# Kernel tuning notes

Measured on AMD Instinct MI355X. Metric: run time of the kernel, lower is better.

Reference implementation:

```python
import jax, jax.numpy as jnp
import numpy as np

N_NODES = 100000
E2 = 1600000
E3 = 1600000
ES = 100000
HID = 64


def _mlp_3x3(x_in, W1, b1, W2, b2):
    # x_in: [E, d_in] -> mobility [E, 3, 3]
    h = jax.nn.relu(x_in @ W1 + b1)
    out = h @ W2 + b2  # [E, 9]
    return out.reshape(-1, 3, 3)


def setup_inputs() -> dict:
    key = jax.random.key(0)
    ks = jax.random.split(key, 20)
    inp = {}
    inp["x"] = jax.random.normal(ks[0], (N_NODES, 3), dtype=jnp.float32)
    inp["edge_2body"] = jax.random.randint(ks[1], (2, E2), 0, N_NODES)
    inp["edge_3body"] = jax.random.randint(ks[2], (3, E3), 0, N_NODES)
    inp["edge_2bodySelf"] = jax.random.randint(ks[3], (2, ES), 0, N_NODES)
    inp["edge_1body"] = jax.random.randint(ks[4], (2, ES), 0, N_NODES)
    inp["edge_attr_2body"] = jax.random.normal(ks[5], (E2, 3), dtype=jnp.float32)
    inp["edge_attr_3body"] = jax.random.normal(ks[6], (E3, 3), dtype=jnp.float32)
    inp["edge_attr_2bodySelf"] = jax.random.normal(ks[7], (ES, 3), dtype=jnp.float32)
    inp["edge_attr_1body"] = jax.random.normal(ks[8], (ES, 3), dtype=jnp.float32)
    s = 0.1
    # nn_2body: 3 -> HID -> 9
    inp["W1_2b"] = jax.random.normal(ks[9], (3, HID), dtype=jnp.float32) * s
    inp["b1_2b"] = jnp.zeros((HID,), jnp.float32)
    inp["W2_2b"] = jax.random.normal(ks[10], (HID, 9), dtype=jnp.float32) * s
    inp["b2_2b"] = jnp.zeros((9,), jnp.float32)
    # nn_3body: 6 -> HID -> 9
    inp["W1_3b"] = jax.random.normal(ks[11], (6, HID), dtype=jnp.float32) * s
    inp["b1_3b"] = jnp.zeros((HID,), jnp.float32)
    inp["W2_3b"] = jax.random.normal(ks[12], (HID, 9), dtype=jnp.float32) * s
    inp["b2_3b"] = jnp.zeros((9,), jnp.float32)
    # nn_self: 3 -> HID -> 9
    inp["W1_s"] = jax.random.normal(ks[13], (3, HID), dtype=jnp.float32) * s
    inp["b1_s"] = jnp.zeros((HID,), jnp.float32)
    inp["W2_s"] = jax.random.normal(ks[14], (HID, 9), dtype=jnp.float32) * s
    inp["b2_s"] = jnp.zeros((9,), jnp.float32)
    return inp


def reference(x, edge_2body, edge_3body, edge_2bodySelf, edge_1body,
              edge_attr_2body, edge_attr_3body, edge_attr_2bodySelf, edge_attr_1body,
              W1_2b, b1_2b, W2_2b, b2_2b,
              W1_3b, b1_3b, W2_3b, b2_3b,
              W1_s, b1_s, W2_s, b2_s):
    n = x.shape[0]
    # ---- 2-body: gather -> MLP -> per-edge 3x3 matvec -> scatter-add ----
    d2 = x[edge_2body[0]] - x[edge_2body[1]]  # xj - xi, [E2,3]
    mob2 = _mlp_3x3(d2, W1_2b, b1_2b, W2_2b, b2_2b)
    y2 = jnp.einsum('eij,ej->ei', mob2, edge_attr_2body)
    v2 = jax.ops.segment_sum(y2, edge_2body[1], num_segments=n)
    # ---- 3-body ----
    xj = x[edge_3body[0]]
    xk = x[edge_3body[1]]
    xi = x[edge_3body[2]]
    d3 = jnp.concatenate((xk - xj, xi - xk), axis=1)  # [E3,6]
    mob3 = _mlp_3x3(d3, W1_3b, b1_3b, W2_3b, b2_3b)
    y3 = jnp.einsum('eij,ej->ei', mob3, edge_attr_3body)
    v3 = jax.ops.segment_sum(y3, edge_3body[2], num_segments=n)
    # ---- 2-body self ----
    ds = x[edge_2bodySelf[0]] - x[edge_2bodySelf[1]]
    mobs = _mlp_3x3(ds, W1_s, b1_s, W2_s, b2_s)
    ys = jnp.einsum('eij,ej->ei', mobs, edge_attr_2bodySelf)
    vs = jax.ops.segment_sum(ys, edge_2bodySelf[1], num_segments=n)
    # edge_1body / edge_attr_1body unused in original forward
    return v2 + v3 + vs
```

## Files before the change

kernel.cpp:

```cpp
#include <hip/hip_runtime.h>


constexpr int HIDDEN = 64;
constexpr int NB_MAX = 256;
constexpr int NPB_SHIFT = 9;
constexpr int NPB = 1 << NPB_SHIFT;
constexpr int TILE_F = NPB * 3;
constexpr int NET_SLOT = 1040;

typedef _Float16 h2_t __attribute__((ext_vector_type(2)));

__device__ __forceinline__ unsigned packh2(float a, float b) {
    auto h = __builtin_amdgcn_cvt_pkrtz(a, b);
    return __builtin_bit_cast(unsigned, h);
}
__device__ __forceinline__ float fdot2u(unsigned a, unsigned b, float c) {
    h2_t ha = __builtin_bit_cast(h2_t, a);
    h2_t hb = __builtin_bit_cast(h2_t, b);
#if __has_builtin(__builtin_amdgcn_fdot2)
    return __builtin_amdgcn_fdot2(ha, hb, c, false);
#else
    return fmaf((float)ha.x, (float)hb.x, fmaf((float)ha.y, (float)hb.y, c));
#endif
}


__global__ __launch_bounds__(256) void setup_kernel(
    const float* __restrict__ x, int n_nodes, float4* __restrict__ x4,
    int* __restrict__ gcount,
    const float* __restrict__ W1_2b, const float* __restrict__ b1_2b,
    const float* __restrict__ W2_2b, const float* __restrict__ b2_2b,
    const float* __restrict__ W1_s,  const float* __restrict__ b1_s,
    const float* __restrict__ W2_s,  const float* __restrict__ b2_s,
    const float* __restrict__ W1_3b, const float* __restrict__ b1_3b,
    const float* __restrict__ W2_3b, const float* __restrict__ b2_3b,
    unsigned* __restrict__ nets)
{
    const int blk = blockIdx.x;
    const int tid = threadIdx.x;
    if (blk < 3) {
        const float *W1, *b1, *W2, *b2; int din;
        if (blk == 0) { W1 = W1_2b; b1 = b1_2b; W2 = W2_2b; b2 = b2_2b; din = 3; }
        else if (blk == 1) { W1 = W1_s; b1 = b1_s; W2 = W2_s; b2 = b2_s; din = 3; }
        else { W1 = W1_3b; b1 = b1_3b; W2 = W2_3b; b2 = b2_3b; din = 6; }
        unsigned* slot = nets + blk * NET_SLOT;
        float* slotf = (float*)slot;
        if (tid < 32) {
            const int h2 = tid, hA = 2 * h2, hB = 2 * h2 + 1;
            if (din == 3) {
                unsigned* row = slot + h2 * 16;
                float* rowf = (float*)row;
                row[0] = packh2(W1[0 * HIDDEN + hA], W1[1 * HIDDEN + hA]);
                row[1] = packh2(W1[0 * HIDDEN + hB], W1[1 * HIDDEN + hB]);
                rowf[2] = b1[hA]; rowf[3] = b1[hB];
                rowf[4] = W1[2 * HIDDEN + hA]; rowf[5] = W1[2 * HIDDEN + hB];
                #pragma unroll
                for (int i = 0; i < 9; ++i)
                    row[6 + i] = packh2(W2[hA * 9 + i], W2[hB * 9 + i]);
                row[15] = 0;
            } else {
                unsigned* row = slot + h2 * 32;
                float* rowf = (float*)row;
                #pragma unroll
                for (int r = 0; r < 3; ++r) {
                    row[r]     = packh2(W1[(2 * r) * HIDDEN + hA], W1[(2 * r + 1) * HIDDEN + hA]);
                    row[3 + r] = packh2(W1[(2 * r) * HIDDEN + hB], W1[(2 * r + 1) * HIDDEN + hB]);
                }
                rowf[6] = b1[hA]; rowf[7] = b1[hB];
                #pragma unroll
                for (int i = 0; i < 9; ++i)
                    row[8 + i] = packh2(W2[hA * 9 + i], W2[hB * 9 + i]);
                #pragma unroll
                for (int i = 17; i < 20; ++i) row[i] = 0;
            }
        }
        if (tid >= 32 && tid < 41) slotf[1024 + (tid - 32)] = b2[tid - 32];
        if (blk == 0) gcount[tid] = 0;
    } else {
        int i = (blk - 3) * 256 + tid;
        if (i < n_nodes)
            x4[i] = make_float4(x[3 * i], x[3 * i + 1], x[3 * i + 2], 0.0f);
    }
}

__global__ __launch_bounds__(256) void p1_edge_kernel(
    const float4* __restrict__ x4,
    const int* __restrict__ e0, long long E0, const float* __restrict__ at0,
    const int* __restrict__ e1, long long E1, const float* __restrict__ at1,
    const int* __restrict__ e2, long long E2, const float* __restrict__ at2,
    int g0, int g1,
    const unsigned* __restrict__ nets,
    float4* __restrict__ records, int* __restrict__ gcount, int cap)
{
    constexpr int BLK = 256;
    constexpr int KPT = 4;
    static_assert(NB_MAX == BLK, "one reserve bin per thread");

    __shared__ int s_hist[NB_MAX];
    __shared__ int s_base[NB_MAX];
    __shared__ int s_rank[NB_MAX];

    const int gA = g0 + g1;
    const int gB = (int)gridDim.x - gA;
    const int mn = (gA < gB) ? gA : gB;
    int aidx = -1, b6 = -1;
    {
        const int idx = blockIdx.x;
        if (idx < 2 * mn) { if (idx & 1) b6 = idx >> 1; else aidx = idx >> 1; }
        else {
            const int r = idx - 2 * mn;
            if (gA > gB) aidx = mn + r; else b6 = mn + r;
        }
    }

    const int* edges; long long E; const float* attr;
    int bidx, nblk, din3;
    const unsigned* wp;
    if (aidx >= 0) {
        if (aidx < g0) { edges = e0; E = E0; attr = at0; bidx = aidx;      nblk = g0; din3 = 1; wp = nets; }
        else           { edges = e1; E = E1; attr = at1; bidx = aidx - g0; nblk = g1; din3 = 1; wp = nets + NET_SLOT; }
    } else             { edges = e2; E = E2; attr = at2; bidx = b6;        nblk = gB; din3 = 0; wp = nets + 2 * NET_SLOT; }

    const int tid = threadIdx.x;
    long long span = (E + nblk - 1) / nblk;
    span = (span + 1023) & ~1023LL;
    const long long lo = (long long)bidx * span;
    const long long hi = (lo + span < E) ? (lo + span) : E;
    if (lo >= E) return;

    const bool e_aligned = ((E & 3) == 0);

    const float* b2f = (const float*)(wp + 1024);
    float b2r[9];
    #pragma unroll
    for (int i = 0; i < 9; ++i) b2r[i] = b2f[i];

    for (int i = tid; i < NB_MAX; i += BLK) { s_hist[i] = 0; s_rank[i] = 0; }
    __syncthreads();

    const long long dstrow = din3 ? E : 2 * E;
    for (long long t0 = lo; t0 < hi; t0 += BLK * KPT) {
        const long long be = t0 + (long long)tid * KPT;
        if (be >= hi) continue;
        if (e_aligned && be + KPT <= hi) {
            int4 r = *(const int4*)(edges + dstrow + be);
            atomicAdd(&s_hist[r.x >> NPB_SHIFT], 1);
            atomicAdd(&s_hist[r.y >> NPB_SHIFT], 1);
            atomicAdd(&s_hist[r.z >> NPB_SHIFT], 1);
            atomicAdd(&s_hist[r.w >> NPB_SHIFT], 1);
        } else {
            #pragma unroll
            for (int u = 0; u < KPT; ++u) {
                long long e = be + u;
                if (e < hi)
                    atomicAdd(&s_hist[edges[dstrow + e] >> NPB_SHIFT], 1);
            }
        }
    }
    __syncthreads();

    int my_base = 0;
    {
        const int h = s_hist[tid];
        if (h > 0) my_base = atomicAdd(&gcount[tid], h);
    }

    bool first = true;
    for (long long t0 = lo; t0 < hi; t0 += BLK * KPT) {
        const long long be = t0 + (long long)tid * KPT;

        unsigned dp[KPT][3];
        float    d2s[KPT];
        float    a[KPT][3];
        int      dst[KPT];
        bool     valid[KPT];
        int      i0[KPT], i1[KPT], i2[KPT];

        const bool full = e_aligned && (be + KPT <= hi);
        if (full) {
            int4 r0 = *(const int4*)(edges + be);
            int4 r1 = *(const int4*)(edges + E + be);
            i0[0] = r0.x; i0[1] = r0.y; i0[2] = r0.z; i0[3] = r0.w;
            i1[0] = r1.x; i1[1] = r1.y; i1[2] = r1.z; i1[3] = r1.w;
            if (!din3) {
                int4 r2 = *(const int4*)(edges + 2 * E + be);
                i2[0] = r2.x; i2[1] = r2.y; i2[2] = r2.z; i2[3] = r2.w;
            }
            float4 a0 = *(const float4*)(attr + 3 * be);
            float4 a1 = *(const float4*)(attr + 3 * be + 4);
            float4 a2 = *(const float4*)(attr + 3 * be + 8);
            a[0][0] = a0.x; a[0][1] = a0.y; a[0][2] = a0.z;
            a[1][0] = a0.w; a[1][1] = a1.x; a[1][2] = a1.y;
            a[2][0] = a1.z; a[2][1] = a1.w; a[2][2] = a2.x;
            a[3][0] = a2.y; a[3][1] = a2.z; a[3][2] = a2.w;
            #pragma unroll
            for (int u = 0; u < KPT; ++u) valid[u] = true;
        } else {
            #pragma unroll
            for (int u = 0; u < KPT; ++u) {
                long long e = be + u;
                valid[u] = (e < hi);
                long long ee = valid[u] ? e : lo;
                i0[u] = edges[ee];
                i1[u] = edges[E + ee];
                if (!din3) i2[u] = edges[2 * E + ee];
                #pragma unroll
                for (int c = 0; c < 3; ++c) a[u][c] = attr[3 * ee + c];
            }
        }

        #pragma unroll
        for (int u = 0; u < KPT; ++u) {
            if (din3) {
                dst[u] = i1[u];
                float4 xs = x4[i0[u]];
                float4 xt = x4[i1[u]];
                dp[u][0] = packh2(xs.x - xt.x, xs.y - xt.y);
                d2s[u]   = xs.z - xt.z;
                dp[u][1] = 0; dp[u][2] = 0;
            } else {
                dst[u] = i2[u];
                float4 xj = x4[i0[u]];
                float4 xk = x4[i1[u]];
                float4 xi = x4[i2[u]];
                dp[u][0] = packh2(xk.x - xj.x, xk.y - xj.y);
                dp[u][1] = packh2(xk.z - xj.z, xi.x - xk.x);
                dp[u][2] = packh2(xi.y - xk.y, xi.z - xk.z);
                d2s[u] = 0.f;
            }
        }

        float acc[KPT][9];
        #pragma unroll
        for (int u = 0; u < KPT; ++u)
            #pragma unroll
            for (int i = 0; i < 9; ++i) acc[u][i] = b2r[i];

        if (din3) {
            #pragma unroll 2
            for (int hh2 = 0; hh2 < HIDDEN / 2; ++hh2) {
                const uint4* rq = (const uint4*)(wp + (hh2 << 4));
                const uint4 q0 = rq[0], q1 = rq[1], q2 = rq[2], q3 = rq[3];
                const unsigned wA = q0.x;
                const unsigned wB = q0.y;
                const float bbA = __uint_as_float(q0.z);
                const float bbB = __uint_as_float(q0.w);
                const float wcA = __uint_as_float(q1.x);
                const float wcB = __uint_as_float(q1.y);
                const unsigned w2p[9] = {q1.z, q1.w, q2.x, q2.y, q2.z,
                                         q2.w, q3.x, q3.y, q3.z};
                #pragma unroll
                for (int u = 0; u < KPT; ++u) {
                    float preA = fmaf(d2s[u], wcA, fdot2u(dp[u][0], wA, bbA));
                    float preB = fmaf(d2s[u], wcB, fdot2u(dp[u][0], wB, bbB));
                    unsigned h2 = packh2(fmaxf(preA, 0.f), fmaxf(preB, 0.f));
                    #pragma unroll
                    for (int i = 0; i < 9; ++i)
                        acc[u][i] = fdot2u(h2, w2p[i], acc[u][i]);
                }
            }
        } else {
            #pragma unroll 2
            for (int hh2 = 0; hh2 < HIDDEN / 2; ++hh2) {
                const uint4* rq = (const uint4*)(wp + (hh2 << 5));
                const uint4 q0 = rq[0], q1 = rq[1], q2 = rq[2], q3 = rq[3];
                const unsigned q4x = wp[(hh2 << 5) + 16];
                const unsigned wA0 = q0.x, wA1 = q0.y, wA2 = q0.z;
                const unsigned wB0 = q0.w, wB1 = q1.x, wB2 = q1.y;
                const float bbA = __uint_as_float(q1.z);
                const float bbB = __uint_as_float(q1.w);
                const unsigned w2p[9] = {q2.x, q2.y, q2.z, q2.w, q3.x,
                                         q3.y, q3.z, q3.w, q4x};
                #pragma unroll
                for (int u = 0; u < KPT; ++u) {
                    float preA = fdot2u(dp[u][2], wA2,
                                 fdot2u(dp[u][1], wA1,
                                 fdot2u(dp[u][0], wA0, bbA)));
                    float preB = fdot2u(dp[u][2], wB2,
                                 fdot2u(dp[u][1], wB1,
                                 fdot2u(dp[u][0], wB0, bbB)));
                    unsigned h2 = packh2(fmaxf(preA, 0.f), fmaxf(preB, 0.f));
                    #pragma unroll
                    for (int i = 0; i < 9; ++i)
                        acc[u][i] = fdot2u(h2, w2p[i], acc[u][i]);
                }
            }
        }

        if (first) {
            s_base[tid] = my_base;
            __syncthreads();
            first = false;
        }

        #pragma unroll
        for (int u = 0; u < KPT; ++u) {
            if (!valid[u]) continue;
            float y0 = fmaf(acc[u][0], a[u][0], fmaf(acc[u][1], a[u][1], acc[u][2] * a[u][2]));
            float y1 = fmaf(acc[u][3], a[u][0], fmaf(acc[u][4], a[u][1], acc[u][5] * a[u][2]));
            float y2 = fmaf(acc[u][6], a[u][0], fmaf(acc[u][7], a[u][1], acc[u][8] * a[u][2]));
            int b = dst[u] >> NPB_SHIFT;
            int r = atomicAdd(&s_rank[b], 1);
            int slot = s_base[b] + r;
            if (slot < cap)
                records[(size_t)b * cap + slot] =
                    make_float4(y0, y1, y2, __int_as_float(dst[u]));
        }
    }
}

__global__ __launch_bounds__(1024) void p2_bucket(
    const float4* __restrict__ records, const int* __restrict__ gcount,
    int cap, int n_nodes, float* __restrict__ out)
{
    __shared__ float s_acc[TILE_F];
    const int b = blockIdx.x;
    const int tid = threadIdx.x;

    for (int i = tid; i < TILE_F; i += 1024) s_acc[i] = 0.0f;
    __syncthreads();

    int cnt = gcount[b];
    if (cnt > cap) cnt = cap;
    const float4* rb = records + (size_t)b * cap;
    for (int i = tid; i < cnt; i += 1024) {
        float4 r = rb[i];
        int loc = __float_as_int(r.w) - (b << NPB_SHIFT);
        atomicAdd(&s_acc[loc * 3 + 0], r.x);
        atomicAdd(&s_acc[loc * 3 + 1], r.y);
        atomicAdd(&s_acc[loc * 3 + 2], r.z);
    }
    __syncthreads();

    const int start = (b << NPB_SHIFT) * 3;
    const int end = min(n_nodes * 3, ((b + 1) << NPB_SHIFT) * 3);
    for (int i = start + tid; i < end; i += 1024)
        out[i] = s_acc[i - start];
}

template <int DIN, int KPT>
__global__ __launch_bounds__(256) void edge_mlp_atomic(
    const float* __restrict__ x,
    const int* __restrict__ edges, long long E,
    const float* __restrict__ attr,
    const float* __restrict__ W1, const float* __restrict__ b1,
    const float* __restrict__ W2, const float* __restrict__ b2,
    float* __restrict__ out)
{
    const int tid = threadIdx.x;
    const long long base = (long long)blockIdx.x * (blockDim.x * KPT) + tid;
    float d[KPT][DIN]; float a[KPT][3]; int dst[KPT]; bool valid[KPT];
    #pragma unroll
    for (int u = 0; u < KPT; ++u) {
        long long e = base + (long long)u * blockDim.x;
        valid[u] = (e < E);
        long long ee = valid[u] ? e : 0;
        if constexpr (DIN == 3) {
            int s = edges[ee]; int t = edges[E + ee]; dst[u] = t;
            #pragma unroll
            for (int c = 0; c < 3; ++c)
                d[u][c] = x[3 * (long long)s + c] - x[3 * (long long)t + c];
        } else {
            int j = edges[ee]; int k = edges[E + ee]; int i = edges[2 * E + ee];
            dst[u] = i;
            #pragma unroll
            for (int c = 0; c < 3; ++c) {
                float xj = x[3 * (long long)j + c];
                float xk = x[3 * (long long)k + c];
                float xi = x[3 * (long long)i + c];
                d[u][c] = xk - xj; d[u][3 + c] = xi - xk;
            }
        }
        #pragma unroll
        for (int c = 0; c < 3; ++c) a[u][c] = attr[3 * ee + c];
    }
    float acc[KPT][9];
    #pragma unroll
    for (int u = 0; u < KPT; ++u)
        #pragma unroll
        for (int i = 0; i < 9; ++i) acc[u][i] = b2[i];
    #pragma unroll 4
    for (int hh = 0; hh < HIDDEN; ++hh) {
        const float bb = b1[hh];
        float w1r[DIN];
        #pragma unroll
        for (int r = 0; r < DIN; ++r) w1r[r] = W1[r * HIDDEN + hh];
        float w2r[9];
        #pragma unroll
        for (int i = 0; i < 9; ++i) w2r[i] = W2[hh * 9 + i];
        #pragma unroll
        for (int u = 0; u < KPT; ++u) {
            float pre = bb;
            #pragma unroll
            for (int r = 0; r < DIN; ++r) pre = fmaf(d[u][r], w1r[r], pre);
            const float h = fmaxf(pre, 0.0f);
            #pragma unroll
            for (int i = 0; i < 9; ++i) acc[u][i] = fmaf(h, w2r[i], acc[u][i]);
        }
    }
    #pragma unroll
    for (int u = 0; u < KPT; ++u) {
        if (!valid[u]) continue;
        float* o = out + 3 * (long long)dst[u];
        #pragma unroll
        for (int i = 0; i < 3; ++i) {
            float y = fmaf(acc[u][3 * i + 0], a[u][0],
                      fmaf(acc[u][3 * i + 1], a[u][1],
                           acc[u][3 * i + 2] * a[u][2]));
            atomicAdd(&o[i], y);
        }
    }
}

extern "C" void kernel_launch(void* const* d_in, const int* in_sizes, int n_in,
                              void* d_out, int out_size, void* d_ws, size_t ws_size,
                              hipStream_t stream)
{
    const float* x  = (const float*)d_in[0];
    const int*   e2 = (const int*)d_in[1];
    const int*   e3 = (const int*)d_in[2];
    const int*   es = (const int*)d_in[3];
    const float* a2 = (const float*)d_in[5];
    const float* a3 = (const float*)d_in[6];
    const float* as = (const float*)d_in[7];
    const float* W1_2b = (const float*)d_in[9];
    const float* b1_2b = (const float*)d_in[10];
    const float* W2_2b = (const float*)d_in[11];
    const float* b2_2b = (const float*)d_in[12];
    const float* W1_3b = (const float*)d_in[13];
    const float* b1_3b = (const float*)d_in[14];
    const float* W2_3b = (const float*)d_in[15];
    const float* b2_3b = (const float*)d_in[16];
    const float* W1_s  = (const float*)d_in[17];
    const float* b1_s  = (const float*)d_in[18];
    const float* W2_s  = (const float*)d_in[19];
    const float* b2_s  = (const float*)d_in[20];

    const long long E2 = in_sizes[1] / 2;
    const long long E3 = in_sizes[2] / 3;
    const long long ES = in_sizes[3] / 2;
    const long long Etot = E2 + E3 + ES;
    const int n_nodes = out_size / 3;
    const int nbuckets = (n_nodes + NPB - 1) >> NPB_SHIFT;

    float* out = (float*)d_out;

    const size_t off_nets = 1024;
    const size_t off_x4 = off_nets + 3 * NET_SLOT * 4;
    const size_t x4_bytes = (size_t)n_nodes * sizeof(float4);
    const size_t off_rec = (off_x4 + x4_bytes + 255) & ~(size_t)255;

    long long mean_per_bucket = (Etot + nbuckets - 1) / nbuckets;
    long long min_cap = mean_per_bucket + 1600;
    long long cap_avail =
        ((long long)ws_size - (long long)off_rec) / ((long long)nbuckets * 16);

    constexpr int SPAN = 2048;
    int g0 = (int)((E2 + SPAN - 1) / SPAN);
    int g1 = (int)((ES + SPAN - 1) / SPAN);
    int g2g = (int)((E3 + SPAN - 1) / SPAN);

    if (nbuckets <= NB_MAX && cap_avail >= min_cap) {
        long long capL = min_cap + 4096;
        if (capL > cap_avail) capL = cap_avail;
        int cap = (int)capL;
        int* gcount = (int*)d_ws;
        unsigned* nets = (unsigned*)((char*)d_ws + off_nets);
        float4* x4 = (float4*)((char*)d_ws + off_x4);
        float4* records = (float4*)((char*)d_ws + off_rec);

        int nb_pad = (n_nodes + 255) / 256;
        setup_kernel<<<3 + nb_pad, 256, 0, stream>>>(
            x, n_nodes, x4, gcount,
            W1_2b, b1_2b, W2_2b, b2_2b,
            W1_s,  b1_s,  W2_s,  b2_s,
            W1_3b, b1_3b, W2_3b, b2_3b,
            nets);

        p1_edge_kernel<<<g0 + g1 + g2g, 256, 0, stream>>>(
            x4,
            e2, E2, a2,
            es, ES, as,
            e3, E3, a3,
            g0, g1,
            nets, records, gcount, cap);

        p2_bucket<<<nbuckets, 1024, 0, stream>>>(records, gcount, cap, n_nodes, out);
    } else {
        hipMemsetAsync(out, 0, (size_t)out_size * sizeof(float), stream);
        constexpr int BLK = 256, KPT = 4;
        const long long per_blk = (long long)BLK * KPT;
        int a2g = (int)((E2 + per_blk - 1) / per_blk);
        int a3g = (int)((E3 + per_blk - 1) / per_blk);
        int asg = (int)((ES + per_blk - 1) / per_blk);
        if (a2g > 0)
            edge_mlp_atomic<3, KPT><<<a2g, BLK, 0, stream>>>(
                x, e2, E2, a2, W1_2b, b1_2b, W2_2b, b2_2b, out);
        if (a3g > 0)
            edge_mlp_atomic<6, KPT><<<a3g, BLK, 0, stream>>>(
                x, e3, E3, a3, W1_3b, b1_3b, W2_3b, b2_3b, out);
        if (asg > 0)
            edge_mlp_atomic<3, KPT><<<asg, BLK, 0, stream>>>(
                x, es, ES, as, W1_s, b1_s, W2_s, b2_s, out);
    }
}
```

Baseline: 334.6 us.

## Stage MLP weights in LDS, split bucket reduction across blocks, halve edge span

The edge kernel now copies its per-network packed weights into shared memory once per block and reads them from LDS in the hidden-unit loop instead of from global memory. The bucket reduction kernel is split into PSPLIT blocks of 512 threads per bucket, and each block atomically adds its partial tile to the output, which the setup kernel now zeroes. The edge span per block is halved to launch more blocks. This aims to raise parallelism in the reduction, which had only about 196 blocks, and to cut global weight traffic. In exchange it adds global float atomics, repeats the per-bucket tile setup four times, and makes the summation order nondeterministic.

```diff
diff --git a/kernel.cpp b/kernel.cpp
--- a/kernel.cpp
+++ b/kernel.cpp
@@ -7,6 +7,7 @@
 constexpr int NPB = 1 << NPB_SHIFT;
 constexpr int TILE_F = NPB * 3;
 constexpr int NET_SLOT = 1040;
+constexpr int PSPLIT = 4;
 
 typedef _Float16 h2_t __attribute__((ext_vector_type(2)));
 
@@ -27,7 +28,7 @@
 
 __global__ __launch_bounds__(256) void setup_kernel(
     const float* __restrict__ x, int n_nodes, float4* __restrict__ x4,
-    int* __restrict__ gcount,
+    int* __restrict__ gcount, float* __restrict__ out,
     const float* __restrict__ W1_2b, const float* __restrict__ b1_2b,
     const float* __restrict__ W2_2b, const float* __restrict__ b2_2b,
     const float* __restrict__ W1_s,  const float* __restrict__ b1_s,
@@ -78,8 +79,12 @@
         if (blk == 0) gcount[tid] = 0;
     } else {
         int i = (blk - 3) * 256 + tid;
-        if (i < n_nodes)
+        if (i < n_nodes) {
             x4[i] = make_float4(x[3 * i], x[3 * i + 1], x[3 * i + 2], 0.0f);
+            out[3 * i + 0] = 0.0f;
+            out[3 * i + 1] = 0.0f;
+            out[3 * i + 2] = 0.0f;
+        }
     }
 }
 
@@ -99,6 +104,7 @@
     __shared__ int s_hist[NB_MAX];
     __shared__ int s_base[NB_MAX];
     __shared__ int s_rank[NB_MAX];
+    __shared__ __align__(16) unsigned s_net[1033];
 
     const int gA = g0 + g1;
     const int gB = (int)gridDim.x - gA;
@@ -130,13 +136,18 @@
 
     const bool e_aligned = ((E & 3) == 0);
 
-    const float* b2f = (const float*)(wp + 1024);
+    for (int i = tid; i < NB_MAX; i += BLK) { s_hist[i] = 0; s_rank[i] = 0; }
+    const int nstage = din3 ? 512 : 1024;
+    for (int i = tid; i < nstage; i += BLK) s_net[i] = wp[i];
+    if (tid < 9) s_net[1024 + tid] = wp[1024 + tid];
+    __syncthreads();
+
+    const unsigned* w = s_net;
+    const float* wf = (const float*)s_net;
+
     float b2r[9];
     #pragma unroll
-    for (int i = 0; i < 9; ++i) b2r[i] = b2f[i];
-
-    for (int i = tid; i < NB_MAX; i += BLK) { s_hist[i] = 0; s_rank[i] = 0; }
-    __syncthreads();
+    for (int i = 0; i < 9; ++i) b2r[i] = wf[1024 + i];
 
     const long long dstrow = din3 ? E : 2 * E;
     for (long long t0 = lo; t0 < hi; t0 += BLK * KPT) {
@@ -239,7 +250,7 @@
         if (din3) {
             #pragma unroll 2
             for (int hh2 = 0; hh2 < HIDDEN / 2; ++hh2) {
-                const uint4* rq = (const uint4*)(wp + (hh2 << 4));
+                const uint4* rq = (const uint4*)(w + (hh2 << 4));
                 const uint4 q0 = rq[0], q1 = rq[1], q2 = rq[2], q3 = rq[3];
                 const unsigned wA = q0.x;
                 const unsigned wB = q0.y;
@@ -262,9 +273,9 @@
         } else {
             #pragma unroll 2
             for (int hh2 = 0; hh2 < HIDDEN / 2; ++hh2) {
-                const uint4* rq = (const uint4*)(wp + (hh2 << 5));
+                const uint4* rq = (const uint4*)(w + (hh2 << 5));
                 const uint4 q0 = rq[0], q1 = rq[1], q2 = rq[2], q3 = rq[3];
-                const unsigned q4x = wp[(hh2 << 5) + 16];
+                const unsigned q4x = w[(hh2 << 5) + 16];
                 const unsigned wA0 = q0.x, wA1 = q0.y, wA2 = q0.z;
                 const unsigned wB0 = q0.w, wB1 = q1.x, wB2 = q1.y;
                 const float bbA = __uint_as_float(q1.z);
@@ -309,21 +320,22 @@
     }
 }
 
-__global__ __launch_bounds__(1024) void p2_bucket(
+__global__ __launch_bounds__(512) void p2_bucket(
     const float4* __restrict__ records, const int* __restrict__ gcount,
     int cap, int n_nodes, float* __restrict__ out)
 {
     __shared__ float s_acc[TILE_F];
-    const int b = blockIdx.x;
+    const int b = blockIdx.x / PSPLIT;
+    const int part = blockIdx.x % PSPLIT;
     const int tid = threadIdx.x;
 
-    for (int i = tid; i < TILE_F; i += 1024) s_acc[i] = 0.0f;
+    for (int i = tid; i < TILE_F; i += 512) s_acc[i] = 0.0f;
     __syncthreads();
 
     int cnt = gcount[b];
     if (cnt > cap) cnt = cap;
     const float4* rb = records + (size_t)b * cap;
-    for (int i = tid; i < cnt; i += 1024) {
+    for (int i = part * 512 + tid; i < cnt; i += 512 * PSPLIT) {
         float4 r = rb[i];
         int loc = __float_as_int(r.w) - (b << NPB_SHIFT);
         atomicAdd(&s_acc[loc * 3 + 0], r.x);
@@ -334,8 +346,10 @@
 
     const int start = (b << NPB_SHIFT) * 3;
     const int end = min(n_nodes * 3, ((b + 1) << NPB_SHIFT) * 3);
-    for (int i = start + tid; i < end; i += 1024)
-        out[i] = s_acc[i - start];
+    for (int i = start + tid; i < end; i += 512) {
+        float v = s_acc[i - start];
+        if (v != 0.0f) atomicAdd(&out[i], v);
+    }
 }
 
 template <int DIN, int KPT>
@@ -455,7 +469,7 @@
     long long cap_avail =
         ((long long)ws_size - (long long)off_rec) / ((long long)nbuckets * 16);
 
-    constexpr int SPAN = 2048;
+    constexpr int SPAN = 1024;
     int g0 = (int)((E2 + SPAN - 1) / SPAN);
     int g1 = (int)((ES + SPAN - 1) / SPAN);
     int g2g = (int)((E3 + SPAN - 1) / SPAN);
@@ -471,7 +485,7 @@
 
         int nb_pad = (n_nodes + 255) / 256;
         setup_kernel<<<3 + nb_pad, 256, 0, stream>>>(
-            x, n_nodes, x4, gcount,
+            x, n_nodes, x4, gcount, out,
             W1_2b, b1_2b, W2_2b, b2_2b,
             W1_s,  b1_s,  W2_s,  b2_s,
             W1_3b, b1_3b, W2_3b, b2_3b,
@@ -485,7 +499,7 @@
             g0, g1,
             nets, records, gcount, cap);
 
-        p2_bucket<<<nbuckets, 1024, 0, stream>>>(records, gcount, cap, n_nodes, out);
+        p2_bucket<<<nbuckets * PSPLIT, 512, 0, stream>>>(records, gcount, cap, n_nodes, out);
     } else {
         hipMemsetAsync(out, 0, (size_t)out_size * sizeof(float), stream);
         constexpr int BLK = 256, KPT = 4;
```

New measurement: 313.0 us. -6.5%, faster.

## Fuse bucket reduction into edge kernel via last-blocks completion counter

Applied to the files above, without the earlier changes.

The separate p2_bucket launch is removed. The last nbuckets blocks to finish in the edge kernel spin until every block has arrived on a global done counter, then each one reduces one bucket of records into shared memory and writes it to the output. The per-block span drops to 1024 edges, so each block runs a single pass. That removes the separate histogram pre-pass: ranks come from shared atomics on the computed destinations, and bucket bases are reserved afterwards. MLP weights are staged into LDS. The change removes one kernel launch and one extra read of the edge indices, but the spin-wait assumes forward progress of earlier blocks, and the final reduction now runs with only 256 threads per bucket.

```diff
diff --git a/kernel.cpp b/kernel.cpp
--- a/kernel.cpp
+++ b/kernel.cpp
@@ -7,6 +7,8 @@
 constexpr int NPB = 1 << NPB_SHIFT;
 constexpr int TILE_F = NPB * 3;
 constexpr int NET_SLOT = 1040;
+constexpr int BLK = 256;
+constexpr int KPT = 4;
 
 typedef _Float16 h2_t __attribute__((ext_vector_type(2)));
 
@@ -75,7 +77,10 @@
             }
         }
         if (tid >= 32 && tid < 41) slotf[1024 + (tid - 32)] = b2[tid - 32];
-        if (blk == 0) gcount[tid] = 0;
+        if (blk == 0) {
+            gcount[tid] = 0;
+            if (tid == 0) gcount[256] = 0;
+        }
     } else {
         int i = (blk - 3) * 256 + tid;
         if (i < n_nodes)
@@ -90,15 +95,20 @@
     const int* __restrict__ e2, long long E2, const float* __restrict__ at2,
     int g0, int g1,
     const unsigned* __restrict__ nets,
-    float4* __restrict__ records, int* __restrict__ gcount, int cap)
+    float4* __restrict__ records, int* __restrict__ gcount, int cap,
+    int nbuckets, int n_nodes, float* __restrict__ out)
 {
-    constexpr int BLK = 256;
-    constexpr int KPT = 4;
     static_assert(NB_MAX == BLK, "one reserve bin per thread");
-
-    __shared__ int s_hist[NB_MAX];
-    __shared__ int s_base[NB_MAX];
-    __shared__ int s_rank[NB_MAX];
+    __shared__ union {
+        struct {
+            __align__(16) unsigned net[1033];
+            int rank[NB_MAX]; int base[NB_MAX];
+        } p1;
+        __align__(16) float acc[TILE_F];
+    } sh;
+    __shared__ int s_done;
+
+    int* gdone = gcount + 256;
 
     const int gA = g0 + g1;
     const int gB = (int)gridDim.x - gA;
@@ -126,48 +136,24 @@
     span = (span + 1023) & ~1023LL;
     const long long lo = (long long)bidx * span;
     const long long hi = (lo + span < E) ? (lo + span) : E;
-    if (lo >= E) return;
-
-    const bool e_aligned = ((E & 3) == 0);
-
-    const float* b2f = (const float*)(wp + 1024);
-    float b2r[9];
-    #pragma unroll
-    for (int i = 0; i < 9; ++i) b2r[i] = b2f[i];
-
-    for (int i = tid; i < NB_MAX; i += BLK) { s_hist[i] = 0; s_rank[i] = 0; }
-    __syncthreads();
-
-    const long long dstrow = din3 ? E : 2 * E;
-    for (long long t0 = lo; t0 < hi; t0 += BLK * KPT) {
-        const long long be = t0 + (long long)tid * KPT;
-        if (be >= hi) continue;
-        if (e_aligned && be + KPT <= hi) {
-            int4 r = *(const int4*)(edges + dstrow + be);
-            atomicAdd(&s_hist[r.x >> NPB_SHIFT], 1);
-            atomicAdd(&s_hist[r.y >> NPB_SHIFT], 1);
-            atomicAdd(&s_hist[r.z >> NPB_SHIFT], 1);
-            atomicAdd(&s_hist[r.w >> NPB_SHIFT], 1);
-        } else {
-            #pragma unroll
-            for (int u = 0; u < KPT; ++u) {
-                long long e = be + u;
-                if (e < hi)
-                    atomicAdd(&s_hist[edges[dstrow + e] >> NPB_SHIFT], 1);
-            }
-        }
-    }
-    __syncthreads();
-
-    int my_base = 0;
-    {
-        const int h = s_hist[tid];
-        if (h > 0) my_base = atomicAdd(&gcount[tid], h);
-    }
-
-    bool first = true;
-    for (long long t0 = lo; t0 < hi; t0 += BLK * KPT) {
-        const long long be = t0 + (long long)tid * KPT;
+    const bool has_work = (lo < E);
+
+    if (has_work) {
+        const bool e_aligned = ((E & 3) == 0);
+
+        sh.p1.rank[tid] = 0;
+        const int nstage = din3 ? 512 : 1024;
+        for (int i = tid; i < nstage; i += BLK) sh.p1.net[i] = wp[i];
+        if (tid < 9) sh.p1.net[1024 + tid] = wp[1024 + tid];
+        __syncthreads();
+
+        const unsigned* w = sh.p1.net;
+        const float* wf = (const float*)sh.p1.net;
+        float b2r[9];
+        #pragma unroll
+        for (int i = 0; i < 9; ++i) b2r[i] = wf[1024 + i];
+
+        const long long be = lo + (long long)tid * KPT;
 
         unsigned dp[KPT][3];
         float    d2s[KPT];
@@ -176,7 +162,8 @@
         bool     valid[KPT];
         int      i0[KPT], i1[KPT], i2[KPT];
 
-        const bool full = e_aligned && (be + KPT <= hi);
+        const bool lane_live = (be < hi);
+        const bool full = lane_live && e_aligned && (be + KPT <= hi);
         if (full) {
             int4 r0 = *(const int4*)(edges + be);
             int4 r1 = *(const int4*)(edges + E + be);
@@ -199,7 +186,7 @@
             #pragma unroll
             for (int u = 0; u < KPT; ++u) {
                 long long e = be + u;
-                valid[u] = (e < hi);
+                valid[u] = lane_live && (e < hi);
                 long long ee = valid[u] ? e : lo;
                 i0[u] = edges[ee];
                 i1[u] = edges[E + ee];
@@ -239,7 +226,7 @@
         if (din3) {
             #pragma unroll 2
             for (int hh2 = 0; hh2 < HIDDEN / 2; ++hh2) {
-                const uint4* rq = (const uint4*)(wp + (hh2 << 4));
+                const uint4* rq = (const uint4*)(w + (hh2 << 4));
                 const uint4 q0 = rq[0], q1 = rq[1], q2 = rq[2], q3 = rq[3];
                 const unsigned wA = q0.x;
                 const unsigned wB = q0.y;
@@ -262,9 +249,9 @@
         } else {
             #pragma unroll 2
             for (int hh2 = 0; hh2 < HIDDEN / 2; ++hh2) {
-                const uint4* rq = (const uint4*)(wp + (hh2 << 5));
+                const uint4* rq = (const uint4*)(w + (hh2 << 5));
                 const uint4 q0 = rq[0], q1 = rq[1], q2 = rq[2], q3 = rq[3];
-                const unsigned q4x = wp[(hh2 << 5) + 16];
+                const unsigned q4x = w[(hh2 << 5) + 16];
                 const unsigned wA0 = q0.x, wA1 = q0.y, wA2 = q0.z;
                 const unsigned wB0 = q0.w, wB1 = q1.x, wB2 = q1.y;
                 const float bbA = __uint_as_float(q1.z);
@@ -287,11 +274,21 @@
             }
         }
 
-        if (first) {
-            s_base[tid] = my_base;
-            __syncthreads();
-            first = false;
-        }
+        int rk[KPT]; int bb[KPT];
+        #pragma unroll
+        for (int u = 0; u < KPT; ++u) {
+            if (valid[u]) {
+                bb[u] = dst[u] >> NPB_SHIFT;
+                rk[u] = atomicAdd(&sh.p1.rank[bb[u]], 1);
+            }
+        }
+        __syncthreads();
+
+        {
+            int c = sh.p1.rank[tid];
+            sh.p1.base[tid] = (c > 0) ? atomicAdd(&gcount[tid], c) : 0;
+        }
+        __syncthreads();
 
         #pragma unroll
         for (int u = 0; u < KPT; ++u) {
@@ -299,46 +296,49 @@
             float y0 = fmaf(acc[u][0], a[u][0], fmaf(acc[u][1], a[u][1], acc[u][2] * a[u][2]));
             float y1 = fmaf(acc[u][3], a[u][0], fmaf(acc[u][4], a[u][1], acc[u][5] * a[u][2]));
             float y2 = fmaf(acc[u][6], a[u][0], fmaf(acc[u][7], a[u][1], acc[u][8] * a[u][2]));
-            int b = dst[u] >> NPB_SHIFT;
-            int r = atomicAdd(&s_rank[b], 1);
-            int slot = s_base[b] + r;
+            int slot = sh.p1.base[bb[u]] + rk[u];
             if (slot < cap)
-                records[(size_t)b * cap + slot] =
+                records[(size_t)bb[u] * cap + slot] =
                     make_float4(y0, y1, y2, __int_as_float(dst[u]));
         }
     }
+
+    __threadfence();
+    if (tid == 0) s_done = atomicAdd(gdone, 1) + 1;
+    __syncthreads();
+    const int T = (int)gridDim.x;
+    const int myord = s_done;
+    if (myord > T - nbuckets) {
+        const int b = myord - (T - nbuckets) - 1;
+        if (tid == 0) {
+            while (__hip_atomic_load(gdone, __ATOMIC_ACQUIRE,
+                                     __HIP_MEMORY_SCOPE_AGENT) < T)
+                __builtin_amdgcn_s_sleep(8);
+        }
+        __syncthreads();
+        __threadfence();
+
+        for (int i = tid; i < TILE_F; i += BLK) sh.acc[i] = 0.0f;
+        __syncthreads();
+        int cnt = gcount[b];
+        if (cnt > cap) cnt = cap;
+        const float4* rb = records + (size_t)b * cap;
+        for (int i = tid; i < cnt; i += BLK) {
+            float4 r = rb[i];
+            int loc = __float_as_int(r.w) - (b << NPB_SHIFT);
+            atomicAdd(&sh.acc[loc * 3 + 0], r.x);
+            atomicAdd(&sh.acc[loc * 3 + 1], r.y);
+            atomicAdd(&sh.acc[loc * 3 + 2], r.z);
+        }
+        __syncthreads();
+        const int start = (b << NPB_SHIFT) * 3;
+        const int end = min(n_nodes * 3, start + TILE_F);
+        for (int i = start + tid; i < end; i += BLK)
+            out[i] = sh.acc[i - start];
+    }
 }
 
-__global__ __launch_bounds__(1024) void p2_bucket(
-    const float4* __restrict__ records, const int* __restrict__ gcount,
-    int cap, int n_nodes, float* __restrict__ out)
-{
-    __shared__ float s_acc[TILE_F];
-    const int b = blockIdx.x;
-    const int tid = threadIdx.x;
-
-    for (int i = tid; i < TILE_F; i += 1024) s_acc[i] = 0.0f;
-    __syncthreads();
-
-    int cnt = gcount[b];
-    if (cnt > cap) cnt = cap;
-    const float4* rb = records + (size_t)b * cap;
-    for (int i = tid; i < cnt; i += 1024) {
-        float4 r = rb[i];
-        int loc = __float_as_int(r.w) - (b << NPB_SHIFT);
-        atomicAdd(&s_acc[loc * 3 + 0], r.x);
-        atomicAdd(&s_acc[loc * 3 + 1], r.y);
-        atomicAdd(&s_acc[loc * 3 + 2], r.z);
-    }
-    __syncthreads();
-
-    const int start = (b << NPB_SHIFT) * 3;
-    const int end = min(n_nodes * 3, ((b + 1) << NPB_SHIFT) * 3);
-    for (int i = start + tid; i < end; i += 1024)
-        out[i] = s_acc[i - start];
-}
-
-template <int DIN, int KPT>
+template <int DIN, int KPTF>
 __global__ __launch_bounds__(256) void edge_mlp_atomic(
     const float* __restrict__ x,
     const int* __restrict__ edges, long long E,
@@ -348,10 +348,10 @@
     float* __restrict__ out)
 {
     const int tid = threadIdx.x;
-    const long long base = (long long)blockIdx.x * (blockDim.x * KPT) + tid;
-    float d[KPT][DIN]; float a[KPT][3]; int dst[KPT]; bool valid[KPT];
+    const long long base = (long long)blockIdx.x * (blockDim.x * KPTF) + tid;
+    float d[KPTF][DIN]; float a[KPTF][3]; int dst[KPTF]; bool valid[KPTF];
     #pragma unroll
-    for (int u = 0; u < KPT; ++u) {
+    for (int u = 0; u < KPTF; ++u) {
         long long e = base + (long long)u * blockDim.x;
         valid[u] = (e < E);
         long long ee = valid[u] ? e : 0;
@@ -374,9 +374,9 @@
         #pragma unroll
         for (int c = 0; c < 3; ++c) a[u][c] = attr[3 * ee + c];
     }
-    float acc[KPT][9];
+    float acc[KPTF][9];
     #pragma unroll
-    for (int u = 0; u < KPT; ++u)
+    for (int u = 0; u < KPTF; ++u)
         #pragma unroll
         for (int i = 0; i < 9; ++i) acc[u][i] = b2[i];
     #pragma unroll 4
@@ -389,7 +389,7 @@
         #pragma unroll
         for (int i = 0; i < 9; ++i) w2r[i] = W2[hh * 9 + i];
         #pragma unroll
-        for (int u = 0; u < KPT; ++u) {
+        for (int u = 0; u < KPTF; ++u) {
             float pre = bb;
             #pragma unroll
             for (int r = 0; r < DIN; ++r) pre = fmaf(d[u][r], w1r[r], pre);
@@ -399,7 +399,7 @@
         }
     }
     #pragma unroll
-    for (int u = 0; u < KPT; ++u) {
+    for (int u = 0; u < KPTF; ++u) {
         if (!valid[u]) continue;
         float* o = out + 3 * (long long)dst[u];
         #pragma unroll
@@ -445,8 +445,8 @@
 
     float* out = (float*)d_out;
 
-    const size_t off_nets = 1024;
-    const size_t off_x4 = off_nets + 3 * NET_SLOT * 4;
+    const size_t off_nets = 2048;
+    const size_t off_x4 = (off_nets + 3 * NET_SLOT * 4 + 255) & ~(size_t)255;
     const size_t x4_bytes = (size_t)n_nodes * sizeof(float4);
     const size_t off_rec = (off_x4 + x4_bytes + 255) & ~(size_t)255;
 
@@ -455,12 +455,13 @@
     long long cap_avail =
         ((long long)ws_size - (long long)off_rec) / ((long long)nbuckets * 16);
 
-    constexpr int SPAN = 2048;
+    constexpr int SPAN = 1024;
     int g0 = (int)((E2 + SPAN - 1) / SPAN);
     int g1 = (int)((ES + SPAN - 1) / SPAN);
     int g2g = (int)((E3 + SPAN - 1) / SPAN);
-
-    if (nbuckets <= NB_MAX && cap_avail >= min_cap) {
+    const int T = g0 + g1 + g2g;
+
+    if (nbuckets <= NB_MAX && cap_avail >= min_cap && T >= nbuckets + 1) {
         long long capL = min_cap + 4096;
         if (capL > cap_avail) capL = cap_avail;
         int cap = (int)capL;
@@ -477,30 +478,29 @@
             W1_3b, b1_3b, W2_3b, b2_3b,
             nets);
 
-        p1_edge_kernel<<<g0 + g1 + g2g, 256, 0, stream>>>(
+        p1_edge_kernel<<<T, 256, 0, stream>>>(
             x4,
             e2, E2, a2,
             es, ES, as,
             e3, E3, a3,
             g0, g1,
-            nets, records, gcount, cap);
-
-        p2_bucket<<<nbuckets, 1024, 0, stream>>>(records, gcount, cap, n_nodes, out);
+            nets, records, gcount, cap,
+            nbuckets, n_nodes, out);
     } else {
         hipMemsetAsync(out, 0, (size_t)out_size * sizeof(float), stream);
-        constexpr int BLK = 256, KPT = 4;
-        const long long per_blk = (long long)BLK * KPT;
+        constexpr int FB_BLK = 256, FB_KPT = 4;
+        const long long per_blk = (long long)FB_BLK * FB_KPT;
         int a2g = (int)((E2 + per_blk - 1) / per_blk);
         int a3g = (int)((E3 + per_blk - 1) / per_blk);
         int asg = (int)((ES + per_blk - 1) / per_blk);
         if (a2g > 0)
-            edge_mlp_atomic<3, KPT><<<a2g, BLK, 0, stream>>>(
+            edge_mlp_atomic<3, FB_KPT><<<a2g, FB_BLK, 0, stream>>>(
                 x, e2, E2, a2, W1_2b, b1_2b, W2_2b, b2_2b, out);
         if (a3g > 0)
-            edge_mlp_atomic<6, KPT><<<a3g, BLK, 0, stream>>>(
+            edge_mlp_atomic<6, FB_KPT><<<a3g, FB_BLK, 0, stream>>>(
                 x, e3, E3, a3, W1_3b, b1_3b, W2_3b, b2_3b, out);
         if (asg > 0)
-            edge_mlp_atomic<3, KPT><<<asg, BLK, 0, stream>>>(
+            edge_mlp_atomic<3, FB_KPT><<<asg, FB_BLK, 0, stream>>>(
                 x, es, ES, as, W1_s, b1_s, W2_s, b2_s, out);
     }
 }
```

Result: slower. 865.3 us (+158.6%).
